# Performance work log

Hardware: AMD Instinct MI355X
Metric: run time of the kernel (lower is better)

The kernel has to match this reference:

```python
import jax, jax.numpy as jnp
import numpy as np

B, L, IN = 4, 2048, 64
D, N, K, NL, NC = 256, 16, 32, 2, 2


def _ln(x, g, b):
    m = x.mean(-1, keepdims=True)
    v = ((x - m) ** 2).mean(-1, keepdims=True)
    return (x - m) * jax.lax.rsqrt(v + 1e-5) * g + b


def _dwconv(x, w, b):
    # depthwise conv1d, kernel 3, padding 1; x: [B,L,D], w: [D,3]
    xp = jnp.pad(x, ((0, 0), (1, 1), (0, 0)))
    return xp[:, :-2] * w[:, 0] + xp[:, 1:-1] * w[:, 1] + xp[:, 2:] * w[:, 2] + b


def _ssm(x, loglam, wd, bd, wb, wc, wo, bo):
    # x: [B,L,D]
    lam = jax.nn.softplus(loglam)                      # [D,N]
    delta = jax.nn.softplus(x @ wd + bd)[..., None]    # [B,L,D,1]
    Bt = (x @ wb)[:, :, None, :]                       # [B,L,1,N]
    Ct = (x @ wc)[:, :, None, :]                       # [B,L,1,N]
    A_d = jnp.exp(-delta * lam)                        # [B,L,D,N]
    B_d = delta * Bt                                   # [B,L,D,N]
    A_l = jnp.moveaxis(A_d, 1, 0)                      # [L,B,D,N]
    B_l = jnp.moveaxis(B_d, 1, 0)

    def step(h, ab):
        a, b = ab
        h = a * h + b
        return h, h

    h0 = jnp.zeros((x.shape[0], D, N), x.dtype)
    _, hs = jax.lax.scan(step, h0, (A_l, B_l))         # [L,B,D,N]
    ys = hs * jnp.moveaxis(Ct, 1, 0)                   # [L,B,D,N]
    out = jnp.moveaxis(ys, 0, 1).reshape(x.shape[0], x.shape[1], D * N)
    return out @ wo + bo


def _temporal_block(x, lg, lb, cw, cb, loglam, wd, bd, wb, wc, wo, bo, gw, gb, pw, pb):
    res = x
    xn = _ln(x, lg, lb)
    xc = _dwconv(xn, cw, cb)
    xs = _ssm(xc, loglam, wd, bd, wb, wc, wo, bo)
    g = jax.nn.sigmoid(xn @ gw + gb)
    return (xs * g) @ pw + pb + res


def _spectral(x, fr, fi):
    X = jnp.fft.rfft(x, axis=1)                        # [B,F,D] complex64
    mag = jnp.abs(X).mean(axis=(0, 2))                 # [F]
    k = min(K, X.shape[1])
    _, idx = jax.lax.top_k(mag, k)
    filt = (fr[:, :k] + 1j * fi[:, :k]).T              # [k,D]
    Xk = X[:, idx, :] * filt[None]
    Xo = jnp.zeros(X.shape, X.dtype).at[:, idx, :].set(Xk)
    return jnp.fft.irfft(Xo, n=x.shape[1], axis=1)


def setup_inputs() -> dict:
    key = jax.random.key(0)
    ks = jax.random.split(key, 32)
    rn = lambda i, shape, s=0.02: jax.random.normal(ks[i], shape, jnp.float32) * s
    inp = {
        "x": jax.random.normal(ks[0], (B, L, IN), jnp.float32),
        "w_in": rn(1, (IN, D), 0.1), "b_in": jnp.zeros((D,), jnp.float32),
        "ln_g": jnp.ones((NL, D), jnp.float32), "ln_b": jnp.zeros((NL, D), jnp.float32),
        "conv_w": rn(2, (NL, D, 3), 0.3), "conv_b": jnp.zeros((NL, D), jnp.float32),
        "loglam": jax.random.uniform(ks[3], (NL, D, N), jnp.float32),
        "wd": rn(4, (NL, D, D), 0.05), "bd": jnp.zeros((NL, D), jnp.float32),
        "wb": rn(5, (NL, D, N), 0.05), "wc": rn(6, (NL, D, N), 0.05),
        "wo": rn(7, (NL, D * N, D), 0.01), "bo": jnp.zeros((NL, D), jnp.float32),
        "gate_w": rn(8, (NL, D, D), 0.05), "gate_b": jnp.zeros((NL, D), jnp.float32),
        "proj_w": rn(9, (NL, D, D), 0.05), "proj_b": jnp.zeros((NL, D), jnp.float32),
        "fr": rn(10, (D, K)), "fi": rn(11, (D, K)),
        "alpha": jnp.full((D,), 0.5, jnp.float32), "beta": jnp.full((D,), 0.5, jnp.float32),
        "g_out": jnp.ones((D,), jnp.float32), "b_out": jnp.zeros((D,), jnp.float32),
        "hw1": rn(12, (D, D // 2), 0.05), "hb1": jnp.zeros((D // 2,), jnp.float32),
        "hw2": rn(13, (D // 2, NC), 0.05), "hb2": jnp.zeros((NC,), jnp.float32),
    }
    return inp


def reference(x, w_in, b_in, ln_g, ln_b, conv_w, conv_b, loglam, wd, bd, wb, wc, wo, bo,
              gate_w, gate_b, proj_w, proj_b, fr, fi, alpha, beta, g_out, b_out,
              hw1, hb1, hw2, hb2):
    h = x @ w_in + b_in                                # [B,L,D]
    xt = h
    for i in range(NL):
        xt = _temporal_block(xt, ln_g[i], ln_b[i], conv_w[i], conv_b[i], loglam[i],
                             wd[i], bd[i], wb[i], wc[i], wo[i], bo[i],
                             gate_w[i], gate_b[i], proj_w[i], proj_b[i])
    xs = _spectral(h, fr, fi)
    z = alpha * xt + beta * xs
    z = _ln(z, g_out, b_out)
    zl = z[:, -1, :]                                   # [B,D]
    hid = jax.nn.silu(zl @ hw1 + hb1)                  # dropout is identity in eval
    return hid @ hw2 + hb2                             # [B,NC]
```

## Files before the change

### kernel.cpp

```cpp
#include <hip/hip_runtime.h>
#include <hip/hip_bf16.h>
#include <math.h>

#define BB   4
#define LL   2048
#define INF_ 64
#define DD   256
#define NN   16
#define KK   32
#define BLn  (BB*LL)
#define FCNT 1025
#define FSTR 1056
#define SKM  8192
#define SKN  256
#define PSZ  ((size_t)SKM * SKN)
#define IX(x) ((x) + ((x) >> 6))
#define SWZ(c, r) ((c) ^ (((r) & 3) << 3))

typedef short short4v __attribute__((ext_vector_type(4)));
typedef short short8 __attribute__((ext_vector_type(8)));
typedef float f32x4  __attribute__((ext_vector_type(4)));

__device__ __forceinline__ float softplusf(float x) {
    return x > 20.f ? x : log1pf(__expf(x));
}
__device__ __forceinline__ float sigmoidf_(float x) {
    return 1.f / (1.f + __expf(-x));
}
__device__ __forceinline__ short bfs(float v) {
    __hip_bfloat16 h = __float2bfloat16(v);
    return *reinterpret_cast<short*>(&h);
}
#define RAWBAR() do { asm volatile("s_waitcnt lgkmcnt(0)" ::: "memory"); \
                      __builtin_amdgcn_s_barrier(); } while (0)

__global__ void prep_kernel(const float* __restrict__ wd, const float* __restrict__ gw,
                            const float* __restrict__ pw, const float* __restrict__ wo,
                            const float* __restrict__ wb, const float* __restrict__ wc,
                            const float* __restrict__ w_in, float* __restrict__ tab,
                            __hip_bfloat16* __restrict__ cat0, __hip_bfloat16* __restrict__ cat1,
                            __hip_bfloat16* __restrict__ gwt, __hip_bfloat16* __restrict__ pwt,
                            __hip_bfloat16* __restrict__ wot, __hip_bfloat16* __restrict__ wint) {
    __shared__ float t[32][33];
    const int tid = threadIdx.x;
    int blk = blockIdx.x;
    if (blk < 8) {
        int i = blk * 256 + tid;
        if (i < 2048) {
            double ang = 2.0 * 3.14159265358979323846 * (double)i / 2048.0;
            tab[i]        = (float)cos(ang);
            tab[2048 + i] = (float)sin(ang);
        }
        return;
    }
    blk -= 8;
    const float* W; __hip_bfloat16* Wt; int K, N, bx, by;
    if (blk < 64)        { W = wd;                     Wt = cat0; K = 256;  N = 256; bx = blk & 7; by = blk >> 3; }
    else if (blk < 128)  { int q = blk - 64;  W = wd + 65536; Wt = cat1; K = 256; N = 256; bx = q & 7; by = q >> 3; }
    else if (blk < 192)  { int q = blk - 128; W = gw;  Wt = gwt;  K = 256;  N = 256; bx = q & 7; by = q >> 3; }
    else if (blk < 256)  { int q = blk - 192; W = pw;  Wt = pwt;  K = 256;  N = 256; bx = q & 7; by = q >> 3; }
    else if (blk < 1280) { int q = blk - 256; W = wo;  Wt = wot;  K = 4096; N = 256; bx = q & 7; by = q >> 3; }
    else if (blk < 1344) {
        int j = (blk - 1280) & 31;
        const float* src0 = (blk < 1312) ? wb : wb + DD * NN;
        const float* src1 = (blk < 1312) ? wc : wc + DD * NN;
        __hip_bfloat16* cat = (blk < 1312) ? cat0 : cat1;
        const float* src = (j < 16) ? src0 : src1;
        cat[(size_t)(256 + j) * 256 + tid] = __float2bfloat16(src[tid * 16 + (j & 15)]);
        return;
    } else { int q = blk - 1344; W = w_in; Wt = wint; K = 64; N = 256; bx = q & 7; by = q >> 3; }
    const int k0 = by * 32, n0 = bx * 32;
    if (k0 >= K) return;
    const int tx = tid & 31, ty = tid >> 5;
    for (int r = ty; r < 32; r += 8) t[r][tx] = W[(size_t)(k0 + r) * N + n0 + tx];
    __syncthreads();
    for (int r = ty; r < 32; r += 8)
        Wt[(size_t)(n0 + r) * K + k0 + tx] = __float2bfloat16(t[tx][r]);
}

__global__ __launch_bounds__(256)
void gemm_in_kernel(const float* __restrict__ x, const __hip_bfloat16* __restrict__ wint,
                    const float* __restrict__ b_in, float* __restrict__ h,
                    float* __restrict__ ht) {
    __shared__ alignas(16) short As[64][72];
    __shared__ alignas(16) short Bs[64][72];
    __shared__ float ts[64][68];
    const int tid = threadIdx.x;
    const int w = tid >> 6, lane = tid & 63;
    const int hi = lane >> 4, lo = lane & 15;
    const int row0 = blockIdx.y * 64, col0 = blockIdx.x * 64;
    const short* B = (const short*)wint;
#pragma unroll
    for (int e = 0; e < 4; ++e) {
        int q = e * 256 + tid;
        int r = q >> 4, c4 = (q & 15) * 4;
        float4 v = *(const float4*)&x[(size_t)(row0 + r) * 64 + c4];
        short4v s = {bfs(v.x), bfs(v.y), bfs(v.z), bfs(v.w)};
        *(short4v*)&As[r][c4] = s;
    }
#pragma unroll
    for (int e = 0; e < 2; ++e) {
        int q = e * 256 + tid;
        int r = q >> 3, c8 = (q & 7) * 8;
        *(short8*)&Bs[r][c8] = *(const short8*)&B[(size_t)(col0 + r) * 64 + c8];
    }
    __syncthreads();
    f32x4 acc[4];
    f32x4 zz = {0.f, 0.f, 0.f, 0.f};
#pragma unroll
    for (int n = 0; n < 4; ++n) acc[n] = zz;
#pragma unroll
    for (int s = 0; s < 2; ++s) {
        short8 af = *(const short8*)&As[w * 16 + lo][s * 32 + hi * 8];
#pragma unroll
        for (int n = 0; n < 4; ++n) {
            short8 bf = *(const short8*)&Bs[n * 16 + lo][s * 32 + hi * 8];
            acc[n] = __builtin_amdgcn_mfma_f32_16x16x32_bf16(af, bf, acc[n], 0, 0, 0);
        }
    }
#pragma unroll
    for (int n = 0; n < 4; ++n)
#pragma unroll
        for (int r = 0; r < 4; ++r) {
            const int row = row0 + w * 16 + hi * 4 + r;
            const int col = col0 + n * 16 + lo;
            float v = acc[n][r] + b_in[col];
            h[(size_t)row * 256 + col] = v;
            ts[n * 16 + lo][w * 16 + hi * 4 + r] = v;
        }
    __syncthreads();
    const int b = row0 >> 11, l0 = row0 & 2047, d0 = col0;
    const int dr = tid >> 2, seg = tid & 3;
    float* dst = ht + ((size_t)(b * 256 + d0 + dr)) * LL + l0 + seg * 16;
#pragma unroll
    for (int j = 0; j < 4; ++j)
        *(f32x4*)&dst[j * 4] = *(const f32x4*)&ts[dr][seg * 16 + j * 4];
}

__global__ __launch_bounds__(256)
void lnconv_kernel(const float* __restrict__ X, const float* __restrict__ g,
                   const float* __restrict__ bln, const float* __restrict__ cw,
                   const float* __restrict__ cb, __hip_bfloat16* __restrict__ xn_bf,
                   __hip_bfloat16* __restrict__ xc_bf) {
    __shared__ float xs[34][260];
    const int tid = threadIdx.x;
    const int w = tid >> 6, lane = tid & 63;
    const int blk = blockIdx.x;
    const int b = (blk * 32) >> 11, L0 = (blk * 32) & 2047;
    const float4 g4 = *(const float4*)&g[lane * 4];
    const float4 b4 = *(const float4*)&bln[lane * 4];
    for (int slot = w; slot < 34; slot += 4) {
        const int l = L0 - 1 + slot;
        if (l < 0 || l >= LL) {
            f32x4 z = {0.f, 0.f, 0.f, 0.f};
            *(f32x4*)&xs[slot][lane * 4] = z;
            continue;
        }
        float4 v = *(const float4*)&X[((size_t)b * LL + l) * DD + lane * 4];
        float s = v.x + v.y + v.z + v.w;
#pragma unroll
        for (int off = 1; off < 64; off <<= 1) s += __shfl_xor(s, off);
        float m = s * (1.f / DD);
        float cx = v.x - m, cy = v.y - m, cz = v.z - m, cw_ = v.w - m;
        float q = cx * cx + cy * cy + cz * cz + cw_ * cw_;
#pragma unroll
        for (int off = 1; off < 64; off <<= 1) q += __shfl_xor(q, off);
        float inv = rsqrtf(q * (1.f / DD) + 1e-5f);
        f32x4 y;
        y[0] = cx * inv * g4.x + b4.x;
        y[1] = cy * inv * g4.y + b4.y;
        y[2] = cz * inv * g4.z + b4.z;
        y[3] = cw_ * inv * g4.w + b4.w;
        *(f32x4*)&xs[slot][lane * 4] = y;
        if (slot >= 1 && slot <= 32) {
            short4v s4 = {bfs(y[0]), bfs(y[1]), bfs(y[2]), bfs(y[3])};
            *(short4v*)&xn_bf[((size_t)b * LL + l) * DD + lane * 4] = s4;
        }
    }
    __syncthreads();
    const int d = tid;
    const float w0 = cw[d * 3 + 0], w1 = cw[d * 3 + 1], w2 = cw[d * 3 + 2], cbd = cb[d];
    float xm = xs[0][d], x0 = xs[1][d];
    for (int rw = 0; rw < 32; ++rw) {
        float xp = xs[rw + 2][d];
        xc_bf[((size_t)b * LL + L0 + rw) * DD + d] =
            __float2bfloat16(fmaf(w0, xm, fmaf(w1, x0, fmaf(w2, xp, cbd))));
        xm = x0; x0 = xp;
    }
}

template<int MODE>
__global__ __launch_bounds__(256)
void gemm_core(const short* __restrict__ A, const short* __restrict__ Bw,
               const float* __restrict__ bias, const float* __restrict__ x1,
               const float* __restrict__ x2, float* __restrict__ o0,
               float* __restrict__ o1, float* __restrict__ o2,
               __hip_bfloat16* __restrict__ ob) {
    __shared__ alignas(16) short As[2][64][40];
    __shared__ alignas(16) short Bs[2][64][40];
    const int tid = threadIdx.x;
    const int w = tid >> 6, lane = tid & 63;
    const int hi = lane >> 4, lo = lane & 15;
    const int row0 = blockIdx.y * 64, col0 = blockIdx.x * 64;
    f32x4 acc[4];
    f32x4 zz = {0.f, 0.f, 0.f, 0.f};
#pragma unroll
    for (int n = 0; n < 4; ++n) acc[n] = zz;
    const int sr = tid >> 2, scw = SWZ((tid & 3) * 8, tid >> 2);
    const size_t aoff = (size_t)(row0 + sr) * 256 + (tid & 3) * 8;
    const size_t boff = (size_t)(col0 + sr) * 256 + (tid & 3) * 8;
    const int rcol = SWZ(hi * 8, lo);
    short8 a_s0, b_s0, a_s1, b_s1;
#define GC_LOAD0(t) { a_s0 = *(const short8*)&A[aoff + (t) * 32]; \
                      b_s0 = *(const short8*)&Bw[boff + (t) * 32]; }
#define GC_LOAD1(t) { a_s1 = *(const short8*)&A[aoff + (t) * 32]; \
                      b_s1 = *(const short8*)&Bw[boff + (t) * 32]; }
#define GC_WRITE0(buf) { *(short8*)&As[buf][sr][scw] = a_s0; *(short8*)&Bs[buf][sr][scw] = b_s0; }
#define GC_WRITE1(buf) { *(short8*)&As[buf][sr][scw] = a_s1; *(short8*)&Bs[buf][sr][scw] = b_s1; }
#define GC_COMPUTE(buf) { \
        short8 af = *(const short8*)&As[buf][w * 16 + lo][rcol]; \
        short8 bf0 = *(const short8*)&Bs[buf][0 * 16 + lo][rcol]; \
        short8 bf1 = *(const short8*)&Bs[buf][1 * 16 + lo][rcol]; \
        short8 bf2 = *(const short8*)&Bs[buf][2 * 16 + lo][rcol]; \
        short8 bf3 = *(const short8*)&Bs[buf][3 * 16 + lo][rcol]; \
        acc[0] = __builtin_amdgcn_mfma_f32_16x16x32_bf16(af, bf0, acc[0], 0, 0, 0); \
        acc[1] = __builtin_amdgcn_mfma_f32_16x16x32_bf16(af, bf1, acc[1], 0, 0, 0); \
        acc[2] = __builtin_amdgcn_mfma_f32_16x16x32_bf16(af, bf2, acc[2], 0, 0, 0); \
        acc[3] = __builtin_amdgcn_mfma_f32_16x16x32_bf16(af, bf3, acc[3], 0, 0, 0); }
    GC_LOAD0(0); GC_LOAD1(1);
    GC_WRITE0(0);
    RAWBAR();
#pragma unroll
    for (int j = 0; j < 8; j += 2) {
        if (j + 2 < 8) GC_LOAD0(j + 2);
        GC_WRITE1(1);
        GC_COMPUTE(0);
        RAWBAR();
        if (j + 3 < 8) GC_LOAD1(j + 3);
        if (j + 2 < 8) GC_WRITE0(0);
        GC_COMPUTE(1);
        RAWBAR();
    }
#pragma unroll
    for (int n = 0; n < 4; ++n) {
#pragma unroll
        for (int r = 0; r < 4; ++r) {
            const int row = row0 + w * 16 + hi * 4 + r;
            const int col = col0 + n * 16 + lo;
            float v = acc[n][r];
            if constexpr (MODE == 0) {
                if (col < 256)      o0[(size_t)row * 256 + col] = softplusf(v + bias[col]);
                else if (col < 272) o1[(size_t)row * 16 + col - 256] = v;
                else if (col < 288) o2[(size_t)row * 16 + col - 272] = v;
            } else if constexpr (MODE == 1) {
                float gv = sigmoidf_(v + bias[col]);
                size_t idx = (size_t)row * 256 + col;
                float s = x1[idx] + x1[PSZ + idx] + x2[col];
                ob[idx] = __float2bfloat16(gv * s);
            } else {
                o0[(size_t)row * 256 + col] = v + bias[col] + x1[(size_t)row * 256 + col];
            }
        }
    }
}

__global__ __launch_bounds__(256)
void gemm_sk_kernel(const __hip_bfloat16* __restrict__ Abf, const __hip_bfloat16* __restrict__ Wt,
                    float* __restrict__ P) {
    __shared__ alignas(16) short As[2][128][40];
    __shared__ alignas(16) short Bs[2][64][40];
    const int tid = threadIdx.x;
    const int f = blockIdx.x;
    const int xcd = f & 7, slot = f >> 3;
    const int col = slot & 3;
    const int rk = xcd + (slot >> 2) * 8;
    const int row = rk & 63, kb = rk >> 6;
    const int row0 = row * 128, col0 = col * 64;
    const size_t kbase = (size_t)kb * 2048;
    const int w = tid >> 6, lane = tid & 63;
    const int hi = lane >> 4, lo = lane & 15;
    const short* A = (const short*)Abf;
    const short* B = (const short*)Wt;
    f32x4 acc[2][4];
    f32x4 zz = {0.f, 0.f, 0.f, 0.f};
#pragma unroll
    for (int m = 0; m < 2; ++m)
#pragma unroll
        for (int n = 0; n < 4; ++n) acc[m][n] = zz;
    const int ra0 = tid >> 2,          ca0 = (tid & 3) * 8;
    const int ra1 = (256 + tid) >> 2,  ca1 = ((256 + tid) & 3) * 8;
    const int cw0 = SWZ(ca0, ra0), cw1 = SWZ(ca1, ra1);
    const size_t aoff0 = (size_t)(row0 + ra0) * 4096 + kbase + ca0;
    const size_t aoff1 = (size_t)(row0 + ra1) * 4096 + kbase + ca1;
    const size_t boff  = (size_t)(col0 + ra0) * 4096 + kbase + ca0;
    const int rcol = SWZ(hi * 8, lo);
    short8 a0_s0, a1_s0, b_s0, a0_s1, a1_s1, b_s1;
#define SK_LOAD0(t) { size_t k0 = (size_t)(t) * 32; \
        a0_s0 = *(const short8*)&A[aoff0 + k0]; \
        a1_s0 = *(const short8*)&A[aoff1 + k0]; \
        b_s0  = *(const short8*)&B[boff  + k0]; }
#define SK_LOAD1(t) { size_t k0 = (size_t)(t) * 32; \
        a0_s1 = *(const short8*)&A[aoff0 + k0]; \
        a1_s1 = *(const short8*)&A[aoff1 + k0]; \
        b_s1  = *(const short8*)&B[boff  + k0]; }
#define SK_WRITE0(buf) { *(short8*)&As[buf][ra0][cw0] = a0_s0; \
        *(short8*)&As[buf][ra1][cw1] = a1_s0; *(short8*)&Bs[buf][ra0][cw0] = b_s0; }
#define SK_WRITE1(buf) { *(short8*)&As[buf][ra0][cw0] = a0_s1; \
        *(short8*)&As[buf][ra1][cw1] = a1_s1; *(short8*)&Bs[buf][ra0][cw0] = b_s1; }
#define SK_COMPUTE(buf) { \
        short8 af0 = *(const short8*)&As[buf][w * 32 + 0 * 16 + lo][rcol]; \
        short8 af1 = *(const short8*)&As[buf][w * 32 + 1 * 16 + lo][rcol]; \
        short8 bf0 = *(const short8*)&Bs[buf][0 * 16 + lo][rcol]; \
        short8 bf1 = *(const short8*)&Bs[buf][1 * 16 + lo][rcol]; \
        short8 bf2 = *(const short8*)&Bs[buf][2 * 16 + lo][rcol]; \
        short8 bf3 = *(const short8*)&Bs[buf][3 * 16 + lo][rcol]; \
        acc[0][0] = __builtin_amdgcn_mfma_f32_16x16x32_bf16(af0, bf0, acc[0][0], 0, 0, 0); \
        acc[0][1] = __builtin_amdgcn_mfma_f32_16x16x32_bf16(af0, bf1, acc[0][1], 0, 0, 0); \
        acc[0][2] = __builtin_amdgcn_mfma_f32_16x16x32_bf16(af0, bf2, acc[0][2], 0, 0, 0); \
        acc[0][3] = __builtin_amdgcn_mfma_f32_16x16x32_bf16(af0, bf3, acc[0][3], 0, 0, 0); \
        acc[1][0] = __builtin_amdgcn_mfma_f32_16x16x32_bf16(af1, bf0, acc[1][0], 0, 0, 0); \
        acc[1][1] = __builtin_amdgcn_mfma_f32_16x16x32_bf16(af1, bf1, acc[1][1], 0, 0, 0); \
        acc[1][2] = __builtin_amdgcn_mfma_f32_16x16x32_bf16(af1, bf2, acc[1][2], 0, 0, 0); \
        acc[1][3] = __builtin_amdgcn_mfma_f32_16x16x32_bf16(af1, bf3, acc[1][3], 0, 0, 0); }
    SK_LOAD0(0); SK_LOAD1(1);
    SK_WRITE0(0);
    RAWBAR();
    for (int j = 0; j < 64; j += 2) {
        if (j + 2 < 64) SK_LOAD0(j + 2);
        SK_WRITE1(1);
        SK_COMPUTE(0);
        RAWBAR();
        if (j + 3 < 64) SK_LOAD1(j + 3);
        if (j + 2 < 64) SK_WRITE0(0);
        SK_COMPUTE(1);
        RAWBAR();
    }
    float* Pk = P + (size_t)kb * PSZ;
#pragma unroll
    for (int m = 0; m < 2; ++m)
#pragma unroll
        for (int n = 0; n < 4; ++n)
#pragma unroll
            for (int r = 0; r < 4; ++r) {
                int rr = row0 + w * 32 + m * 16 + hi * 4 + r;
                int cc = col0 + n * 16 + lo;
                Pk[(size_t)rr * SKN + cc] = acc[m][n][r];
            }
}

template<int PHASE>
__global__ void ssm_chunk_kernel(const float* __restrict__ delta, const float* __restrict__ Bt,
                                 const float* __restrict__ Ct, const float* __restrict__ loglam,
                                 float* __restrict__ sA, float* __restrict__ sB,
                                 __hip_bfloat16* __restrict__ ys) {
    __shared__ float dl[128][16];
    __shared__ float btl[128][16];
    __shared__ float ctl[128][16];
    const int dblk = blockIdx.x, c = blockIdx.y, b = blockIdx.z;
    const int tid = threadIdx.x;
    const size_t lbase = (size_t)b * LL + c * 128;
    for (int i = tid; i < 2048; i += 256) {
        int l = i >> 4, q = i & 15;
        dl[l][q]  = delta[(lbase + l) * DD + dblk * 16 + q];
        btl[l][q] = Bt[(lbase + l) * NN + q];
        if (PHASE == 1) ctl[l][q] = Ct[(lbase + l) * NN + q];
    }
    float hv = 0.f, ap = 1.f;
    if (PHASE == 1) {
        for (int cc = 0; cc < c; ++cc) {
            size_t oi = ((size_t)(b * 16 + cc)) * 4096 + dblk * 256 + tid;
            hv = fmaf(sA[oi], hv, sB[oi]);
        }
    }
    __syncthreads();
    const int dloc = tid >> 4, n = tid & 15;
    const float lam = softplusf(loglam[(dblk * 16 + dloc) * NN + n]);
    for (int l = 0; l < 128; ++l) {
        float dv = dl[l][dloc];
        float a = __expf(-dv * lam);
        hv = fmaf(a, hv, dv * btl[l][n]);
        if (PHASE == 0) ap *= a;
        else ys[(lbase + l) * (DD * NN) + dblk * 256 + tid] = __float2bfloat16(hv * ctl[l][n]);
    }
    if (PHASE == 0) {
        size_t oi = ((size_t)(b * 16 + c)) * 4096 + dblk * 256 + tid;
        sA[oi] = ap; sB[oi] = hv;
    }
}

__global__ void last_ssm_part_kernel(const float* __restrict__ sA, const float* __restrict__ sB,
                                     const float* __restrict__ Ct,
                                     const float* __restrict__ wo, float* __restrict__ part) {
    __shared__ float hC[4][128];
    const int c = blockIdx.x, tid = threadIdx.x;
    const int p0 = c * 128;
#pragma unroll
    for (int e = 0; e < 2; ++e) {
        int i = e * 256 + tid;
        int b = i >> 7, p = i & 127;
        float hh = 0.f;
#pragma unroll
        for (int cc = 0; cc < 16; ++cc) {
            size_t oi = ((size_t)(b * 16 + cc)) * 4096 + p0 + p;
            hh = fmaf(sA[oi], hh, sB[oi]);
        }
        hC[b][p] = hh * Ct[((size_t)b * LL + (LL - 1)) * NN + (p & 15)];
    }
    __syncthreads();
    float a0 = 0.f, a1 = 0.f, a2 = 0.f, a3 = 0.f;
    for (int p = 0; p < 128; ++p) {
        float wv = wo[(size_t)(p0 + p) * DD + tid];
        a0 = fmaf(hC[0][p], wv, a0);
        a1 = fmaf(hC[1][p], wv, a1);
        a2 = fmaf(hC[2][p], wv, a2);
        a3 = fmaf(hC[3][p], wv, a3);
    }
    part[(0 * 32 + c) * DD + tid] = a0;
    part[(1 * 32 + c) * DD + tid] = a1;
    part[(2 * 32 + c) * DD + tid] = a2;
    part[(3 * 32 + c) * DD + tid] = a3;
}

__global__ void last_redproj_kernel(const float* __restrict__ part, const float* __restrict__ bo,
                                    const __hip_bfloat16* __restrict__ xn, const float* __restrict__ gw,
                                    const float* __restrict__ gb, const float* __restrict__ pw,
                                    const float* __restrict__ pb, const float* __restrict__ resid,
                                    float* __restrict__ xtlast) {
    __shared__ float xrow[256];
    __shared__ float xsg[256];
    const int b = blockIdx.x, d = threadIdx.x;
    float ol = bo[d];
#pragma unroll
    for (int c = 0; c < 32; ++c) ol += part[(b * 32 + c) * DD + d];
    const size_t rbase = ((size_t)b * LL + (LL - 1)) * DD;
    xrow[d] = __bfloat162float(xn[rbase + d]);
    __syncthreads();
    float acc = gb[d];
    for (int k = 0; k < 256; ++k) acc = fmaf(xrow[k], gw[(size_t)k * DD + d], acc);
    xsg[d] = ol * sigmoidf_(acc);
    __syncthreads();
    float acc2 = pb[d];
    for (int k = 0; k < 256; ++k) acc2 = fmaf(xsg[k], pw[(size_t)k * DD + d], acc2);
    xtlast[b * DD + d] = acc2 + resid[rbase + d];
}

__global__ __launch_bounds__(256)
void fft2_kernel(const float* __restrict__ ht, const float* __restrict__ tab,
                 float* __restrict__ Xre, float* __restrict__ Xim) {
    __shared__ float re[2080];
    __shared__ float im[2080];
    __shared__ float c2[2048];
    __shared__ float s2[2048];
    const int tid = threadIdx.x;
    const int pair = blockIdx.x;
    const int b = pair >> 7, d0 = pair & 127;
    for (int p = tid; p < 2048; p += 256) {
        if (p >= 1) {
            int lh = 31 - __clz((unsigned)p);
            int j = p - (1 << lh);
            int t = j << (10 - lh);
            c2[p] = tab[t]; s2[p] = tab[2048 + t];
        }
    }
    const float* ha = ht + ((size_t)b * 256 + d0) * LL;
    const float* hb = ha + (size_t)128 * LL;
    for (int i = tid; i < 2048; i += 256) {
        int r = (int)(__brev((unsigned)i) >> 21);
        re[IX(r)] = ha[i];
        im[IX(r)] = hb[i];
    }
    __syncthreads();
#pragma unroll
    for (int s = 1; s <= 11; ++s) {
        const int half = 1 << (s - 1);
#pragma unroll
        for (int e = 0; e < 4; ++e) {
            int q = e * 256 + tid;
            int j = q & (half - 1);
            int i0 = ((q >> (s - 1)) << s) + j;
            int i1 = i0 + half;
            float wr = c2[half + j], wi = -s2[half + j];
            float xr = re[IX(i1)], xi = im[IX(i1)];
            float tr = xr * wr - xi * wi;
            float ti = xr * wi + xi * wr;
            float ur = re[IX(i0)], ui = im[IX(i0)];
            re[IX(i0)] = ur + tr; im[IX(i0)] = ui + ti;
            re[IX(i1)] = ur - tr; im[IX(i1)] = ui - ti;
        }
        __syncthreads();
    }
    const int seqa = b * 256 + d0;
    float* xra = Xre + (size_t)seqa * FSTR;
    float* xia = Xim + (size_t)seqa * FSTR;
    float* xrb = xra + (size_t)128 * FSTR;
    float* xib = xia + (size_t)128 * FSTR;
    for (int f = tid; f < FCNT; f += 256) {
        int nf = (2048 - f) & 2047;
        float zrf = re[IX(f)], zif = im[IX(f)];
        float zrn = re[IX(nf)], zin = im[IX(nf)];
        xra[f] = 0.5f * (zrf + zrn);
        xia[f] = 0.5f * (zif - zin);
        xrb[f] = 0.5f * (zif + zin);
        xib[f] = 0.5f * (zrn - zrf);
    }
}

__global__ void mag_part_kernel(const float* __restrict__ Xre, const float* __restrict__ Xim,
                                float* __restrict__ part) {
    const int fb = blockIdx.x, sb = blockIdx.y;
    const int tid = threadIdx.x;
    const int f = fb * 256 + tid;
    float s = 0.f;
    if (f < FCNT) {
        for (int q = 0; q < 64; ++q) {
            size_t base = (size_t)(sb * 64 + q) * FSTR + f;
            float re = Xre[base], im = Xim[base];
            s += sqrtf(re * re + im * im);
        }
    }
    part[sb * 1280 + fb * 256 + tid] = s;
}

__global__ void topk_kernel(const float* __restrict__ part, int* __restrict__ sel) {
    __shared__ float vals[1280];
    __shared__ float wval[4][32];
    __shared__ int   widx[4][32];
    const int tid = threadIdx.x;
    const int lane = tid & 63, wid = tid >> 6;
    for (int i = tid; i < 1280; i += 256) {
        float v = -1e30f;
        if (i < FCNT) {
            v = 0.f;
#pragma unroll
            for (int sb = 0; sb < 16; ++sb) v += part[sb * 1280 + i];
        }
        vals[i] = v;
    }
    __syncthreads();
    const int base = wid * 320;
    for (int k = 0; k < 32; ++k) {
        float bv = -1e30f; int bi = 0x7fffffff;
#pragma unroll
        for (int q = 0; q < 5; ++q) {
            int i = base + q * 64 + lane;
            float v = vals[i];
            if (v > bv) { bv = v; bi = i; }
        }
#pragma unroll
        for (int off = 32; off > 0; off >>= 1) {
            float ov = __shfl_down(bv, off);
            int   oi = __shfl_down(bi, off);
            if (ov > bv || (ov == bv && oi < bi)) { bv = ov; bi = oi; }
        }
        bv = __shfl(bv, 0);
        bi = __shfl(bi, 0);
        if (lane == 0) { wval[wid][k] = bv; widx[wid][k] = bi; }
        vals[bi] = -1e30f;
    }
    __syncthreads();
    if (tid == 0) {
        int p0 = 0, p1 = 0, p2 = 0, p3 = 0;
        for (int k = 0; k < 32; ++k) {
            float v0 = wval[0][p0], v1 = wval[1][p1], v2 = wval[2][p2], v3 = wval[3][p3];
            int bw = 0; float bv = v0;
            if (v1 > bv) { bv = v1; bw = 1; }
            if (v2 > bv) { bv = v2; bw = 2; }
            if (v3 > bv) { bv = v3; bw = 3; }
            if (bw == 0)      { sel[k] = widx[0][p0++]; }
            else if (bw == 1) { sel[k] = widx[1][p1++]; }
            else if (bw == 2) { sel[k] = widx[2][p2++]; }
            else              { sel[k] = widx[3][p3++]; }
        }
    }
}

__global__ void head_kernel(const float* __restrict__ Xre, const float* __restrict__ Xim,
                            const int* __restrict__ sel, const float* __restrict__ fr,
                            const float* __restrict__ fi, const float* __restrict__ tab,
                            const float* __restrict__ xtlast,
                            const float* __restrict__ alpha, const float* __restrict__ beta,
                            const float* __restrict__ gout, const float* __restrict__ bout,
                            const float* __restrict__ hw1, const float* __restrict__ hb1,
                            const float* __restrict__ hw2, const float* __restrict__ hb2,
                            float* __restrict__ out) {
    __shared__ float red[256];
    __shared__ float z[256];
    __shared__ float hid[128];
    const int b = blockIdx.x, tid = threadIdx.x;
    const size_t sbase = (size_t)(b * 256 + tid) * FSTR;
    float xsl = 0.f;
    for (int j = 0; j < 32; ++j) {
        int f = sel[j];
        float xr = Xre[sbase + f];
        float xi = Xim[sbase + f];
        float frv = fr[tid * KK + j], fiv = fi[tid * KK + j];
        float xor_ = xr * frv - xi * fiv;
        float xoi  = xr * fiv + xi * frv;
        int kk2 = (f * (LL - 1)) & (LL - 1);
        float c = tab[kk2], s = tab[2048 + kk2];
        float w = (f == 0 || f == 1024) ? 1.f : 2.f;
        xsl = fmaf(w, xor_ * c - xoi * s, xsl);
    }
    xsl *= (1.f / LL);
    float zv = alpha[tid] * xtlast[b * 256 + tid] + beta[tid] * xsl;
    red[tid] = zv; __syncthreads();
    for (int s = 128; s > 0; s >>= 1) { if (tid < s) red[tid] += red[tid + s]; __syncthreads(); }
    float m = red[0] * (1.f / DD);
    __syncthreads();
    float c = zv - m;
    red[tid] = c * c; __syncthreads();
    for (int s = 128; s > 0; s >>= 1) { if (tid < s) red[tid] += red[tid + s]; __syncthreads(); }
    float var = red[0] * (1.f / DD);
    z[tid] = c * rsqrtf(var + 1e-5f) * gout[tid] + bout[tid];
    __syncthreads();
    if (tid < 128) {
        float a = hb1[tid];
        for (int k = 0; k < 256; ++k) a = fmaf(z[k], hw1[(size_t)k * 128 + tid], a);
        hid[tid] = a * sigmoidf_(a);
    }
    __syncthreads();
    if (tid < 2) {
        float a = hb2[tid];
        for (int k = 0; k < 128; ++k) a = fmaf(hid[k], hw2[(size_t)k * 2 + tid], a);
        out[b * 2 + tid] = a;
    }
}

extern "C" void kernel_launch(void* const* d_in, const int* in_sizes, int n_in,
                              void* d_out, int out_size, void* d_ws, size_t ws_size,
                              hipStream_t stream) {
    const float* x      = (const float*)d_in[0];
    const float* w_in   = (const float*)d_in[1];
    const float* b_in   = (const float*)d_in[2];
    const float* ln_g   = (const float*)d_in[3];
    const float* ln_b   = (const float*)d_in[4];
    const float* conv_w = (const float*)d_in[5];
    const float* conv_b = (const float*)d_in[6];
    const float* loglam = (const float*)d_in[7];
    const float* wd     = (const float*)d_in[8];
    const float* bd     = (const float*)d_in[9];
    const float* wb     = (const float*)d_in[10];
    const float* wc     = (const float*)d_in[11];
    const float* wo     = (const float*)d_in[12];
    const float* bo     = (const float*)d_in[13];
    const float* gw     = (const float*)d_in[14];
    const float* gb     = (const float*)d_in[15];
    const float* pw     = (const float*)d_in[16];
    const float* pb     = (const float*)d_in[17];
    const float* fr     = (const float*)d_in[18];
    const float* fi     = (const float*)d_in[19];
    const float* alpha  = (const float*)d_in[20];
    const float* beta   = (const float*)d_in[21];
    const float* gout   = (const float*)d_in[22];
    const float* bout   = (const float*)d_in[23];
    const float* hw1    = (const float*)d_in[24];
    const float* hb1    = (const float*)d_in[25];
    const float* hw2    = (const float*)d_in[26];
    const float* hb2    = (const float*)d_in[27];

    float* ws = (float*)d_ws;
    size_t o = 0;
    auto alloc = [&](size_t n) { float* p = ws + o; o += (n + 15) & ~(size_t)15; return p; };

    const size_t BLnDD = (size_t)BLn * DD;
    float* h      = alloc(BLnDD);
    float* xt1    = alloc(BLnDD);
    float* ht     = alloc(BLnDD);
    float* delta  = alloc(BLnDD);
    float* Pbuf   = alloc(2 * PSZ);
    float* Btm    = alloc((size_t)BLn * NN);
    float* Ctm    = alloc((size_t)BLn * NN);
    float* tab    = alloc(4096);
    float* ysf    = alloc(BLnDD * NN / 2);
    float* sA     = alloc((size_t)BB * 16 * 4096);
    float* sB     = alloc((size_t)BB * 16 * 4096);
    float* xnbf_f = alloc(BLnDD / 2);
    float* xcbf_f = alloc(BLnDD / 2);
    float* xsgf   = alloc(BLnDD / 2);
    float* cat0_f = alloc((size_t)320 * 256 / 2);
    float* cat1_f = alloc((size_t)320 * 256 / 2);
    float* gwt_f  = alloc((size_t)DD * DD / 2);
    float* pwt_f  = alloc((size_t)DD * DD / 2);
    float* wot_f  = alloc((size_t)DD * NN * DD / 2);
    float* wint_f = alloc((size_t)DD * 64 / 2);
    float* magp   = alloc(16 * 1280);
    int*   sel    = (int*)alloc(32);
    float* lpart  = alloc((size_t)BB * 32 * DD);
    float* xtlast = alloc(BB * DD);

    __hip_bfloat16* ys    = (__hip_bfloat16*)ysf;
    float*          Xre   = ysf;
    float*          Xim   = ysf + (size_t)1024 * FSTR;
    __hip_bfloat16* xn_bf = (__hip_bfloat16*)xnbf_f;
    __hip_bfloat16* xc_bf = (__hip_bfloat16*)xcbf_f;
    __hip_bfloat16* xsg_bf= (__hip_bfloat16*)xsgf;
    __hip_bfloat16* cat0  = (__hip_bfloat16*)cat0_f;
    __hip_bfloat16* cat1  = (__hip_bfloat16*)cat1_f;
    __hip_bfloat16* gwt   = (__hip_bfloat16*)gwt_f;
    __hip_bfloat16* pwt   = (__hip_bfloat16*)pwt_f;
    __hip_bfloat16* wot   = (__hip_bfloat16*)wot_f;
    __hip_bfloat16* wint  = (__hip_bfloat16*)wint_f;

    const dim3 blk(256);

    prep_kernel<<<1368, blk, 0, stream>>>(wd, gw, pw, wo, wb, wc, w_in, tab,
                                          cat0, cat1, gwt, pwt, wot, wint);
    gemm_in_kernel<<<dim3(4, 128), blk, 0, stream>>>(x, wint, b_in, h, ht);

    const dim3 qgrid(5, BLn / 64);
    const dim3 ggrid(4, BLn / 64);
    const dim3 sgrid(16, 16, BB);

    lnconv_kernel<<<BLn / 32, blk, 0, stream>>>(h, ln_g, ln_b, conv_w, conv_b, xn_bf, xc_bf);
    gemm_core<0><<<qgrid, blk, 0, stream>>>((const short*)xc_bf, (const short*)cat0,
                                            bd, nullptr, nullptr, delta, Btm, Ctm, nullptr);
    ssm_chunk_kernel<0><<<sgrid, blk, 0, stream>>>(delta, Btm, nullptr, loglam,
                                                   sA, sB, nullptr);
    ssm_chunk_kernel<1><<<sgrid, blk, 0, stream>>>(delta, Btm, Ctm, loglam,
                                                   sA, sB, ys);
    gemm_sk_kernel<<<512, blk, 0, stream>>>(ys, wot, Pbuf);
    gemm_core<1><<<ggrid, blk, 0, stream>>>((const short*)xn_bf, (const short*)gwt,
                                            gb, Pbuf, bo, nullptr, nullptr, nullptr, xsg_bf);
    gemm_core<2><<<ggrid, blk, 0, stream>>>((const short*)xsg_bf, (const short*)pwt,
                                            pb, h, nullptr, xt1, nullptr, nullptr, nullptr);

    lnconv_kernel<<<BLn / 32, blk, 0, stream>>>(xt1, ln_g + DD, ln_b + DD,
                                                conv_w + DD * 3, conv_b + DD, xn_bf, xc_bf);
    gemm_core<0><<<qgrid, blk, 0, stream>>>((const short*)xc_bf, (const short*)cat1,
                                            bd + DD, nullptr, nullptr, delta, Btm, Ctm, nullptr);
    ssm_chunk_kernel<0><<<sgrid, blk, 0, stream>>>(delta, Btm, nullptr, loglam + DD * NN,
                                                   sA, sB, nullptr);
    last_ssm_part_kernel<<<32, blk, 0, stream>>>(sA, sB, Ctm, wo + (size_t)DD * NN * DD, lpart);
    last_redproj_kernel<<<BB, blk, 0, stream>>>(lpart, bo + DD, xn_bf,
                                                gw + (size_t)DD * DD, gb + DD,
                                                pw + (size_t)DD * DD, pb + DD, xt1, xtlast);

    fft2_kernel<<<512, blk, 0, stream>>>(ht, tab, Xre, Xim);
    mag_part_kernel<<<dim3(5, 16), blk, 0, stream>>>(Xre, Xim, magp);
    topk_kernel<<<1, blk, 0, stream>>>(magp, sel);

    head_kernel<<<BB, blk, 0, stream>>>(Xre, Xim, sel, fr, fi, tab, xtlast,
                                        alpha, beta, gout, bout,
                                        hw1, hb1, hw2, hb2, (float*)d_out);
}
```

Before: 280.9 us.

## Rework split-K GEMM to direct-register MFMA tiles with four K splits

```diff
diff --git a/kernel.cpp b/kernel.cpp
--- a/kernel.cpp
+++ b/kernel.cpp
@@ -255,7 +255,7 @@
             } else if constexpr (MODE == 1) {
                 float gv = sigmoidf_(v + bias[col]);
                 size_t idx = (size_t)row * 256 + col;
-                float s = x1[idx] + x1[PSZ + idx] + x2[col];
+                float s = x1[idx] + x1[PSZ + idx] + x1[2 * PSZ + idx] + x1[3 * PSZ + idx] + x2[col];
                 ob[idx] = __float2bfloat16(gv * s);
             } else {
                 o0[(size_t)row * 256 + col] = v + bias[col] + x1[(size_t)row * 256 + col];
@@ -267,82 +267,80 @@
 __global__ __launch_bounds__(256)
 void gemm_sk_kernel(const __hip_bfloat16* __restrict__ Abf, const __hip_bfloat16* __restrict__ Wt,
                     float* __restrict__ P) {
-    __shared__ alignas(16) short As[2][128][40];
-    __shared__ alignas(16) short Bs[2][64][40];
     const int tid = threadIdx.x;
     const int f = blockIdx.x;
-    const int xcd = f & 7, slot = f >> 3;
-    const int col = slot & 3;
-    const int rk = xcd + (slot >> 2) * 8;
-    const int row = rk & 63, kb = rk >> 6;
-    const int row0 = row * 128, col0 = col * 64;
-    const size_t kbase = (size_t)kb * 2048;
+    const int xcd = f & 7, s = f >> 3;
+    const int col = s & 3, u = s >> 2;
+    const int rowkb = xcd + u * 8;
+    const int rowslab = rowkb & 31, kb = rowkb >> 5;
     const int w = tid >> 6, lane = tid & 63;
     const int hi = lane >> 4, lo = lane & 15;
+    const int wrow = rowslab * 256 + w * 64;
+    const int col0 = col * 64;
+    const size_t kbase = (size_t)kb * 1024;
     const short* A = (const short*)Abf;
     const short* B = (const short*)Wt;
-    f32x4 acc[2][4];
+    f32x4 acc[4][4];
     f32x4 zz = {0.f, 0.f, 0.f, 0.f};
 #pragma unroll
-    for (int m = 0; m < 2; ++m)
+    for (int m = 0; m < 4; ++m)
 #pragma unroll
         for (int n = 0; n < 4; ++n) acc[m][n] = zz;
-    const int ra0 = tid >> 2,          ca0 = (tid & 3) * 8;
-    const int ra1 = (256 + tid) >> 2,  ca1 = ((256 + tid) & 3) * 8;
-    const int cw0 = SWZ(ca0, ra0), cw1 = SWZ(ca1, ra1);
-    const size_t aoff0 = (size_t)(row0 + ra0) * 4096 + kbase + ca0;
-    const size_t aoff1 = (size_t)(row0 + ra1) * 4096 + kbase + ca1;
-    const size_t boff  = (size_t)(col0 + ra0) * 4096 + kbase + ca0;
-    const int rcol = SWZ(hi * 8, lo);
-    short8 a0_s0, a1_s0, b_s0, a0_s1, a1_s1, b_s1;
-#define SK_LOAD0(t) { size_t k0 = (size_t)(t) * 32; \
-        a0_s0 = *(const short8*)&A[aoff0 + k0]; \
-        a1_s0 = *(const short8*)&A[aoff1 + k0]; \
-        b_s0  = *(const short8*)&B[boff  + k0]; }
-#define SK_LOAD1(t) { size_t k0 = (size_t)(t) * 32; \
-        a0_s1 = *(const short8*)&A[aoff0 + k0]; \
-        a1_s1 = *(const short8*)&A[aoff1 + k0]; \
-        b_s1  = *(const short8*)&B[boff  + k0]; }
-#define SK_WRITE0(buf) { *(short8*)&As[buf][ra0][cw0] = a0_s0; \
-        *(short8*)&As[buf][ra1][cw1] = a1_s0; *(short8*)&Bs[buf][ra0][cw0] = b_s0; }
-#define SK_WRITE1(buf) { *(short8*)&As[buf][ra0][cw0] = a0_s1; \
-        *(short8*)&As[buf][ra1][cw1] = a1_s1; *(short8*)&Bs[buf][ra0][cw0] = b_s1; }
-#define SK_COMPUTE(buf) { \
-        short8 af0 = *(const short8*)&As[buf][w * 32 + 0 * 16 + lo][rcol]; \
-        short8 af1 = *(const short8*)&As[buf][w * 32 + 1 * 16 + lo][rcol]; \
-        short8 bf0 = *(const short8*)&Bs[buf][0 * 16 + lo][rcol]; \
-        short8 bf1 = *(const short8*)&Bs[buf][1 * 16 + lo][rcol]; \
-        short8 bf2 = *(const short8*)&Bs[buf][2 * 16 + lo][rcol]; \
-        short8 bf3 = *(const short8*)&Bs[buf][3 * 16 + lo][rcol]; \
-        acc[0][0] = __builtin_amdgcn_mfma_f32_16x16x32_bf16(af0, bf0, acc[0][0], 0, 0, 0); \
-        acc[0][1] = __builtin_amdgcn_mfma_f32_16x16x32_bf16(af0, bf1, acc[0][1], 0, 0, 0); \
-        acc[0][2] = __builtin_amdgcn_mfma_f32_16x16x32_bf16(af0, bf2, acc[0][2], 0, 0, 0); \
-        acc[0][3] = __builtin_amdgcn_mfma_f32_16x16x32_bf16(af0, bf3, acc[0][3], 0, 0, 0); \
-        acc[1][0] = __builtin_amdgcn_mfma_f32_16x16x32_bf16(af1, bf0, acc[1][0], 0, 0, 0); \
-        acc[1][1] = __builtin_amdgcn_mfma_f32_16x16x32_bf16(af1, bf1, acc[1][1], 0, 0, 0); \
-        acc[1][2] = __builtin_amdgcn_mfma_f32_16x16x32_bf16(af1, bf2, acc[1][2], 0, 0, 0); \
-        acc[1][3] = __builtin_amdgcn_mfma_f32_16x16x32_bf16(af1, bf3, acc[1][3], 0, 0, 0); }
-    SK_LOAD0(0); SK_LOAD1(1);
-    SK_WRITE0(0);
-    RAWBAR();
-    for (int j = 0; j < 64; j += 2) {
-        if (j + 2 < 64) SK_LOAD0(j + 2);
-        SK_WRITE1(1);
-        SK_COMPUTE(0);
-        RAWBAR();
-        if (j + 3 < 64) SK_LOAD1(j + 3);
-        if (j + 2 < 64) SK_WRITE0(0);
-        SK_COMPUTE(1);
-        RAWBAR();
+    const size_t ao0 = (size_t)(wrow + 0 * 16 + lo) * 4096 + kbase + hi * 8;
+    const size_t ao1 = (size_t)(wrow + 1 * 16 + lo) * 4096 + kbase + hi * 8;
+    const size_t ao2 = (size_t)(wrow + 2 * 16 + lo) * 4096 + kbase + hi * 8;
+    const size_t ao3 = (size_t)(wrow + 3 * 16 + lo) * 4096 + kbase + hi * 8;
+    const size_t bo0 = (size_t)(col0 + 0 * 16 + lo) * 4096 + kbase + hi * 8;
+    const size_t bo1 = (size_t)(col0 + 1 * 16 + lo) * 4096 + kbase + hi * 8;
+    const size_t bo2 = (size_t)(col0 + 2 * 16 + lo) * 4096 + kbase + hi * 8;
+    const size_t bo3 = (size_t)(col0 + 3 * 16 + lo) * 4096 + kbase + hi * 8;
+    short8 aX0, aX1, aX2, aX3, bX0, bX1, bX2, bX3;
+    short8 aY0, aY1, aY2, aY3, bY0, bY1, bY2, bY3;
+#define SK_LOADX(t) { size_t ko = (size_t)(t) * 32; \
+        aX0 = *(const short8*)&A[ao0 + ko]; aX1 = *(const short8*)&A[ao1 + ko]; \
+        aX2 = *(const short8*)&A[ao2 + ko]; aX3 = *(const short8*)&A[ao3 + ko]; \
+        bX0 = *(const short8*)&B[bo0 + ko]; bX1 = *(const short8*)&B[bo1 + ko]; \
+        bX2 = *(const short8*)&B[bo2 + ko]; bX3 = *(const short8*)&B[bo3 + ko]; }
+#define SK_LOADY(t) { size_t ko = (size_t)(t) * 32; \
+        aY0 = *(const short8*)&A[ao0 + ko]; aY1 = *(const short8*)&A[ao1 + ko]; \
+        aY2 = *(const short8*)&A[ao2 + ko]; aY3 = *(const short8*)&A[ao3 + ko]; \
+        bY0 = *(const short8*)&B[bo0 + ko]; bY1 = *(const short8*)&B[bo1 + ko]; \
+        bY2 = *(const short8*)&B[bo2 + ko]; bY3 = *(const short8*)&B[bo3 + ko]; }
+#define MF(a_, b_, c_) __builtin_amdgcn_mfma_f32_16x16x32_bf16(a_, b_, c_, 0, 0, 0)
+#define SK_COMPX() { \
+        acc[0][0]=MF(aX0,bX0,acc[0][0]); acc[0][1]=MF(aX0,bX1,acc[0][1]); \
+        acc[0][2]=MF(aX0,bX2,acc[0][2]); acc[0][3]=MF(aX0,bX3,acc[0][3]); \
+        acc[1][0]=MF(aX1,bX0,acc[1][0]); acc[1][1]=MF(aX1,bX1,acc[1][1]); \
+        acc[1][2]=MF(aX1,bX2,acc[1][2]); acc[1][3]=MF(aX1,bX3,acc[1][3]); \
+        acc[2][0]=MF(aX2,bX0,acc[2][0]); acc[2][1]=MF(aX2,bX1,acc[2][1]); \
+        acc[2][2]=MF(aX2,bX2,acc[2][2]); acc[2][3]=MF(aX2,bX3,acc[2][3]); \
+        acc[3][0]=MF(aX3,bX0,acc[3][0]); acc[3][1]=MF(aX3,bX1,acc[3][1]); \
+        acc[3][2]=MF(aX3,bX2,acc[3][2]); acc[3][3]=MF(aX3,bX3,acc[3][3]); }
+#define SK_COMPY() { \
+        acc[0][0]=MF(aY0,bY0,acc[0][0]); acc[0][1]=MF(aY0,bY1,acc[0][1]); \
+        acc[0][2]=MF(aY0,bY2,acc[0][2]); acc[0][3]=MF(aY0,bY3,acc[0][3]); \
+        acc[1][0]=MF(aY1,bY0,acc[1][0]); acc[1][1]=MF(aY1,bY1,acc[1][1]); \
+        acc[1][2]=MF(aY1,bY2,acc[1][2]); acc[1][3]=MF(aY1,bY3,acc[1][3]); \
+        acc[2][0]=MF(aY2,bY0,acc[2][0]); acc[2][1]=MF(aY2,bY1,acc[2][1]); \
+        acc[2][2]=MF(aY2,bY2,acc[2][2]); acc[2][3]=MF(aY2,bY3,acc[2][3]); \
+        acc[3][0]=MF(aY3,bY0,acc[3][0]); acc[3][1]=MF(aY3,bY1,acc[3][1]); \
+        acc[3][2]=MF(aY3,bY2,acc[3][2]); acc[3][3]=MF(aY3,bY3,acc[3][3]); }
+    SK_LOADX(0);
+    SK_LOADY(1);
+    for (int j = 0; j < 32; j += 2) {
+        SK_COMPX();
+        if (j + 2 < 32) SK_LOADX(j + 2);
+        SK_COMPY();
+        if (j + 3 < 32) SK_LOADY(j + 3);
     }
     float* Pk = P + (size_t)kb * PSZ;
 #pragma unroll
-    for (int m = 0; m < 2; ++m)
+    for (int m = 0; m < 4; ++m)
 #pragma unroll
         for (int n = 0; n < 4; ++n)
 #pragma unroll
             for (int r = 0; r < 4; ++r) {
-                int rr = row0 + w * 32 + m * 16 + hi * 4 + r;
+                int rr = wrow + m * 16 + hi * 4 + r;
                 int cc = col0 + n * 16 + lo;
                 Pk[(size_t)rr * SKN + cc] = acc[m][n][r];
             }
@@ -667,7 +665,7 @@
     float* xt1    = alloc(BLnDD);
     float* ht     = alloc(BLnDD);
     float* delta  = alloc(BLnDD);
-    float* Pbuf   = alloc(2 * PSZ);
+    float* Pbuf   = alloc(4 * PSZ);
     float* Btm    = alloc((size_t)BLn * NN);
     float* Ctm    = alloc((size_t)BLn * NN);
     float* tab    = alloc(4096);
```

New measurement: 304.7 us. 8.4% more time.
